# Kernel optimization log

Hardware: AMD Instinct MI355X
Metric: run time of the kernel (lower is better)

## Reference

```python
import jax, jax.numpy as jnp
import numpy as np

B, C, L, T = 8, 512, 2048, 64

def setup_inputs() -> dict:
    key = jax.random.key(0)
    k1, k2, k3 = jax.random.split(key, 3)
    x = jax.random.normal(k1, (B, C, 1, L), dtype=jnp.float32)
    W1 = jax.random.normal(k2, (T, C), dtype=jnp.float32) * (1.0 / np.sqrt(C))
    W2 = jax.random.normal(k3, (T, C), dtype=jnp.float32) * (1.0 / np.sqrt(C))
    gamma = jnp.ones((1, 1), dtype=jnp.float32)
    ranges = 0  # unused by forward
    return {"x": x, "W1": W1, "W2": W2, "gamma": gamma, "ranges": ranges}

def reference(x, W1, W2, gamma, ranges):
    temp = x[:, :, 0, :]                                  # (B, C, L)
    q = jnp.einsum('tc,bcl->btl', W1, temp)               # conv1x1 -> (B, T, L)
    k = jnp.einsum('tc,bcl->btl', W2, temp)               # conv1x1 -> (B, T, L)
    scores = jnp.einsum('btl,btm->blm', q, k)             # Q^T K -> (B, L, L)
    attn = jax.nn.softmax(scores, axis=2)                 # softmax over last dim
    # temp @ attn^T: out[:, :, j] = sum_i attn[j, i] * temp[:, :, i]
    out = jnp.einsum('bci,bji->bcj', temp, attn)          # (B, C, L)
    out = temp + gamma[0, 0] * out                        # gamma scale + residual
    return out[:, :, None, :]                             # (B, C, 1, L)
```

## Files before the change

kernel.cpp:

```cpp
#include <hip/hip_runtime.h>
#include <cstddef>

#define BB 8
#define CC 512
#define LL 2048
#define TT 64

typedef short short8 __attribute__((ext_vector_type(8)));
typedef float floatx4 __attribute__((ext_vector_type(4)));
typedef unsigned short b16u;
typedef unsigned int u32;

static __device__ __forceinline__ unsigned f2bfu(float f) {
    unsigned u = __float_as_uint(f);
    u += 0x7fffu + ((u >> 16) & 1u);
    return u >> 16;
}
static __device__ __forceinline__ float bfu2f(unsigned h) {
    return __uint_as_float(h << 16);
}

#define MFMA16(a, b, c) __builtin_amdgcn_mfma_f32_16x16x32_bf16((a), (b), (c), 0, 0, 0)

static __device__ __forceinline__ void gl2lds16(const void* g, void* l) {
    __builtin_amdgcn_global_load_lds(
        (const __attribute__((address_space(1))) u32*)g,
        (__attribute__((address_space(3))) u32*)l, 16, 0, 0);
}

__global__ __launch_bounds__(256) void wcvt_kernel(
    const float* __restrict__ W1, const float* __restrict__ W2,
    b16u* __restrict__ W1h, b16u* __restrict__ W1l,
    b16u* __restrict__ W2h, b16u* __restrict__ W2l)
{
    int flat = blockIdx.x * 256 + threadIdx.x;
    float4 v1 = *(const float4*)(W1 + (size_t)flat * 4);
    float4 v2 = *(const float4*)(W2 + (size_t)flat * 4);
    const float* e1 = (const float*)&v1;
    const float* e2 = (const float*)&v2;
    unsigned h1[4], l1[4], h2[4], l2[4];
#pragma unroll
    for (int k = 0; k < 4; ++k) {
        h1[k] = f2bfu(e1[k]); l1[k] = f2bfu(e1[k] - bfu2f(h1[k]));
        h2[k] = f2bfu(e2[k]); l2[k] = f2bfu(e2[k] - bfu2f(h2[k]));
    }
    uint2 a, b, c, d;
    a.x = h1[0] | (h1[1] << 16); a.y = h1[2] | (h1[3] << 16);
    b.x = l1[0] | (l1[1] << 16); b.y = l1[2] | (l1[3] << 16);
    c.x = h2[0] | (h2[1] << 16); c.y = h2[2] | (h2[3] << 16);
    d.x = l2[0] | (l2[1] << 16); d.y = l2[2] | (l2[3] << 16);
    *(uint2*)(W1h + (size_t)flat * 4) = a;
    *(uint2*)(W1l + (size_t)flat * 4) = b;
    *(uint2*)(W2h + (size_t)flat * 4) = c;
    *(uint2*)(W2l + (size_t)flat * 4) = d;
}

__global__ __launch_bounds__(256) void qkcvt_kernel(
    const float* __restrict__ x,
    const b16u* __restrict__ W1h, const b16u* __restrict__ W1l,
    const b16u* __restrict__ W2h, const b16u* __restrict__ W2l,
    b16u* __restrict__ Qt, b16u* __restrict__ Kt, b16u* __restrict__ XT)
{
    __shared__ b16u Sxh[64 * 72];
    __shared__ b16u Sxl[64 * 72];
    __shared__ b16u S1h[64 * 72];
    __shared__ b16u S1l[64 * 72];
    __shared__ b16u S2h[64 * 72];
    __shared__ b16u S2l[64 * 72];
    const int b  = blockIdx.y;
    const int lt = blockIdx.x;
    const int l0 = lt * 64;
    const int tid = threadIdx.x;
    const int lane = tid & 63;
    const int w = tid >> 6;
    const int n16 = lane & 15;
    const int qd = lane >> 4;
    const float* xb = x + (size_t)b * CC * LL;

    const int cx = tid >> 2;
    const int sx = tid & 3;

    float4 xreg[4];
#pragma unroll
    for (int p = 0; p < 4; ++p)
        xreg[p] = *(const float4*)(xb + (size_t)cx * LL + l0 + (sx * 4 + p) * 4);

    floatx4 aq[4], ak[4];
#pragma unroll
    for (int nt = 0; nt < 4; ++nt) {
        aq[nt] = (floatx4){0.f, 0.f, 0.f, 0.f};
        ak[nt] = (floatx4){0.f, 0.f, 0.f, 0.f};
    }

    for (int c0 = 0; c0 < 512; c0 += 64) {
        __syncthreads();
#pragma unroll
        for (int p = 0; p < 4; ++p) {
            const float* e = (const float*)&xreg[p];
            int s = sx * 4 + p;
            int lbase = s * 4;
            unsigned h[4];
#pragma unroll
            for (int k = 0; k < 4; ++k) {
                h[k] = f2bfu(e[k]);
                unsigned lo = f2bfu(e[k] - bfu2f(h[k]));
                Sxh[(lbase + k) * 72 + cx] = (b16u)h[k];
                Sxl[(lbase + k) * 72 + cx] = (b16u)lo;
            }
            uint2 wv;
            wv.x = h[0] | (h[1] << 16);
            wv.y = h[2] | (h[3] << 16);
            int phys = (((s >> 1) ^ (cx & 7)) << 3) + ((s & 1) << 2);
            *(uint2*)(XT + (((size_t)(b * 32) + lt) * 512 + c0 + cx) * 64 + phys) = wv;
        }
#pragma unroll
        for (int p = 0; p < 2; ++p) {
            int flat = tid + p * 256;
            int t = flat >> 3, s8 = flat & 7;
            size_t off = (size_t)t * 512 + c0 + s8 * 8;
            *(uint4*)&S1h[t * 72 + s8 * 8] = *(const uint4*)(W1h + off);
            *(uint4*)&S1l[t * 72 + s8 * 8] = *(const uint4*)(W1l + off);
            *(uint4*)&S2h[t * 72 + s8 * 8] = *(const uint4*)(W2h + off);
            *(uint4*)&S2l[t * 72 + s8 * 8] = *(const uint4*)(W2l + off);
        }
        __syncthreads();
        if (c0 < 448) {
#pragma unroll
            for (int p = 0; p < 4; ++p)
                xreg[p] = *(const float4*)(xb + (size_t)(c0 + 64 + cx) * LL +
                                           l0 + (sx * 4 + p) * 4);
        }
#pragma unroll
        for (int kc = 0; kc < 2; ++kc) {
            const int ao = (w * 16 + n16) * 72 + kc * 32 + qd * 8;
            short8 a1h = *(const short8*)&S1h[ao];
            short8 a1l = *(const short8*)&S1l[ao];
            short8 a2h = *(const short8*)&S2h[ao];
            short8 a2l = *(const short8*)&S2l[ao];
#pragma unroll
            for (int nt = 0; nt < 4; ++nt) {
                const int bo = (nt * 16 + n16) * 72 + kc * 32 + qd * 8;
                short8 bh = *(const short8*)&Sxh[bo];
                short8 bl = *(const short8*)&Sxl[bo];
                aq[nt] = MFMA16(a1h, bh, aq[nt]);
                aq[nt] = MFMA16(a1h, bl, aq[nt]);
                aq[nt] = MFMA16(a1l, bh, aq[nt]);
                ak[nt] = MFMA16(a2h, bh, ak[nt]);
                ak[nt] = MFMA16(a2h, bl, ak[nt]);
                ak[nt] = MFMA16(a2l, bh, ak[nt]);
            }
        }
    }
#pragma unroll
    for (int nt = 0; nt < 4; ++nt) {
        int l = l0 + nt * 16 + n16;
        uint2 pq, pk;
        pq.x = f2bfu(aq[nt][0]) | (f2bfu(aq[nt][1]) << 16);
        pq.y = f2bfu(aq[nt][2]) | (f2bfu(aq[nt][3]) << 16);
        pk.x = f2bfu(ak[nt][0]) | (f2bfu(ak[nt][1]) << 16);
        pk.y = f2bfu(ak[nt][2]) | (f2bfu(ak[nt][3]) << 16);
        *(uint2*)(Qt + ((size_t)(b * 2048) + l) * 64 + w * 16 + qd * 4) = pq;
        *(uint2*)(Kt + ((size_t)(b * 2048) + l) * 64 + w * 16 + qd * 4) = pk;
    }
}

__global__ __launch_bounds__(256) void pexp_kernel(
    const b16u* __restrict__ Qt, const b16u* __restrict__ Kt,
    b16u* __restrict__ P, float* __restrict__ Zpart, int b_off)
{
    __shared__ b16u Ks[64 * 72];
    __shared__ b16u Ls[64 * 68];
    __shared__ float Zw[4][64];
    const int pb = blockIdx.z, b = b_off + pb;
    const int j0 = blockIdx.y * 64;
    const int ibase = blockIdx.x * 512;
    const int tid = threadIdx.x;
    const int lane = tid & 63;
    const int w = tid >> 6;
    const int n16 = lane & 15;
    const int qd = lane >> 4;
    const b16u* kb = Kt + (size_t)b * (2048 * 64);

    short8 qf[4][2];
#pragma unroll
    for (int nt = 0; nt < 4; ++nt)
#pragma unroll
        for (int kc = 0; kc < 2; ++kc)
            qf[nt][kc] = *(const short8*)(Qt +
                ((size_t)(b * 2048) + j0 + nt * 16 + n16) * 64 + kc * 32 + qd * 8);

    uint4 kreg[2];
#pragma unroll
    for (int p = 0; p < 2; ++p) {
        int flat = tid + p * 256;
        kreg[p] = *(const uint4*)(kb + (size_t)(ibase + (flat >> 3)) * 64 + (flat & 7) * 8);
    }
    float zacc[4] = {0.f, 0.f, 0.f, 0.f};

    for (int it = 0; it < 8; ++it) {
#pragma unroll
        for (int p = 0; p < 2; ++p) {
            int flat = tid + p * 256;
            *(uint4*)&Ks[(flat >> 3) * 72 + (flat & 7) * 8] = kreg[p];
        }
        {
            const int itn = (it + 1 < 8) ? it + 1 : 7;
#pragma unroll
            for (int p = 0; p < 2; ++p) {
                int flat = tid + p * 256;
                kreg[p] = *(const uint4*)(kb +
                    (size_t)(ibase + itn * 64 + (flat >> 3)) * 64 + (flat & 7) * 8);
            }
        }
        __syncthreads();
        floatx4 sacc[4];
#pragma unroll
        for (int nt = 0; nt < 4; ++nt) sacc[nt] = (floatx4){0.f, 0.f, 0.f, 0.f};
#pragma unroll
        for (int kc = 0; kc < 2; ++kc) {
            short8 af = *(const short8*)&Ks[(w * 16 + n16) * 72 + kc * 32 + qd * 8];
#pragma unroll
            for (int nt = 0; nt < 4; ++nt)
                sacc[nt] = MFMA16(af, qf[nt][kc], sacc[nt]);
        }
#pragma unroll
        for (int nt = 0; nt < 4; ++nt) {
            float p0 = __expf(sacc[nt][0] - 20.0f);
            float p1 = __expf(sacc[nt][1] - 20.0f);
            float p2 = __expf(sacc[nt][2] - 20.0f);
            float p3 = __expf(sacc[nt][3] - 20.0f);
            zacc[nt] += (p0 + p1) + (p2 + p3);
            uint2 pk;
            pk.x = f2bfu(p0) | (f2bfu(p1) << 16);
            pk.y = f2bfu(p2) | (f2bfu(p3) << 16);
            *(uint2*)&Ls[(nt * 16 + n16) * 68 + w * 16 + qd * 4] = pk;
        }
        __syncthreads();
        size_t prow = ((size_t)(pb * 32) + (ibase >> 6) + it) * 2048 + j0;
#pragma unroll
        for (int p = 0; p < 4; ++p) {
            int u = tid + p * 256;
            int row = u >> 4, s = u & 15;
            int phys = (((s >> 1) ^ (row & 7)) << 3) + ((s & 1) << 2);
            *(uint2*)(P + (prow + row) * 64 + phys) = *(const uint2*)&Ls[row * 68 + s * 4];
        }
    }
#pragma unroll
    for (int nt = 0; nt < 4; ++nt) {
        float z = zacc[nt];
        z += __shfl_xor(z, 16);
        z += __shfl_xor(z, 32);
        if (qd == 0) Zw[w][nt * 16 + n16] = z;
    }
    __syncthreads();
    if (tid < 64) {
        float s = Zw[0][tid] + Zw[1][tid] + Zw[2][tid] + Zw[3][tid];
        Zpart[((size_t)blockIdx.x * 8 + b) * 2048 + j0 + tid] = s;
    }
}

__global__ __launch_bounds__(128) void gemm_kernel(
    const float* __restrict__ x, const b16u* __restrict__ XT,
    const b16u* __restrict__ P, const float* __restrict__ Zpart,
    const float* __restrict__ gamma, float* __restrict__ out, int b_off)
{
    __shared__ __align__(16) char smem[49152];
    b16u* As = (b16u*)smem;
    b16u* Bs = (b16u*)(smem + 32768);
    const int pb = blockIdx.z, b = b_off + pb;
    const int j0 = blockIdx.x * 64;
    const int c0 = blockIdx.y * 128;
    const int tid = threadIdx.x;
    const int lane = tid & 63;
    const int w = tid >> 6;
    const int n16 = lane & 15;
    const int qd = lane >> 4;

    const b16u* tA = XT + ((size_t)(b * 32) * 512 + c0) * 64 + w * 4096 + lane * 8;
    const b16u* tB = P + ((size_t)(pb * 32) * 2048 + j0) * 64 + w * 2048 + lane * 8;
    b16u* lA = As + w * 4096;
    b16u* lB = Bs + w * 2048;

#define STAGE(IT, BUF)                                                    \
    {                                                                      \
        const b16u* ga = tA + (size_t)(IT) * 32768;                        \
        const b16u* gb = tB + (size_t)(IT) * 131072;                       \
        _Pragma("unroll")                                                  \
        for (int ch = 0; ch < 8; ++ch)                                     \
            gl2lds16(ga + ch * 512, lA + (BUF) * 8192 + ch * 512);         \
        _Pragma("unroll")                                                  \
        for (int ch = 0; ch < 4; ++ch)                                     \
            gl2lds16(gb + ch * 512, lB + (BUF) * 4096 + ch * 512);         \
    }

    STAGE(0, 0)
    __syncthreads();

    floatx4 acc[4][4];
#pragma unroll
    for (int mt = 0; mt < 4; ++mt)
#pragma unroll
        for (int nt = 0; nt < 4; ++nt) acc[mt][nt] = (floatx4){0.f, 0.f, 0.f, 0.f};

    for (int it = 0; it < 32; ++it) {
        const int buf = it & 1;
        if (it < 31) STAGE(it + 1, buf ^ 1)
        const b16u* Ab = As + buf * 8192;
        const b16u* Bb = Bs + buf * 4096;
#pragma unroll
        for (int kc = 0; kc < 2; ++kc) {
            const int co = (((kc * 4 + qd) ^ (n16 & 7)) << 3);
            short8 af[4], bf[4];
#pragma unroll
            for (int mt = 0; mt < 4; ++mt)
                af[mt] = *(const short8*)&Ab[(w * 64 + mt * 16 + n16) * 64 + co];
#pragma unroll
            for (int nt = 0; nt < 4; ++nt)
                bf[nt] = *(const short8*)&Bb[(nt * 16 + n16) * 64 + co];
#pragma unroll
            for (int mt = 0; mt < 4; ++mt)
#pragma unroll
                for (int nt = 0; nt < 4; ++nt)
                    acc[mt][nt] = MFMA16(af[mt], bf[nt], acc[mt][nt]);
        }
        __syncthreads();
    }
#undef STAGE

    const float g = gamma[0];
    float* st = (float*)(smem + w * 17408);
#pragma unroll
    for (int nt = 0; nt < 4; ++nt) {
        int j = j0 + nt * 16 + n16;
        float zsum = Zpart[(size_t)b * 2048 + j]
                   + Zpart[(size_t)(1 * 8 + b) * 2048 + j]
                   + Zpart[(size_t)(2 * 8 + b) * 2048 + j]
                   + Zpart[(size_t)(3 * 8 + b) * 2048 + j];
        float zi = g / zsum;
#pragma unroll
        for (int mt = 0; mt < 4; ++mt)
#pragma unroll
            for (int r = 0; r < 4; ++r)
                st[(mt * 16 + qd * 4 + r) * 68 + nt * 16 + n16] = acc[mt][nt][r] * zi;
    }
    __syncthreads();
#pragma unroll
    for (int p = 0; p < 16; ++p) {
        int rl = p * 4 + qd;
        int cg = c0 + w * 64 + rl;
        size_t go = ((size_t)(b * 512) + cg) * 2048 + j0 + n16 * 4;
        float4 v = *(const float4*)&st[rl * 68 + n16 * 4];
        float4 xv = *(const float4*)(x + go);
        v.x += xv.x; v.y += xv.y; v.z += xv.z; v.w += xv.w;
        *(float4*)(out + go) = v;
    }
}

extern "C" void kernel_launch(void* const* d_in, const int* in_sizes, int n_in,
                              void* d_out, int out_size, void* d_ws, size_t ws_size,
                              hipStream_t stream)
{
    const float* x     = (const float*)d_in[0];
    const float* W1    = (const float*)d_in[1];
    const float* W2    = (const float*)d_in[2];
    const float* gamma = (const float*)d_in[3];
    float* out = (float*)d_out;

    b16u* Qt  = (b16u*)d_ws;
    b16u* Kt  = Qt  + (size_t)BB * LL * TT;
    b16u* W1h = Kt  + (size_t)BB * LL * TT;
    b16u* W1l = W1h + (size_t)TT * CC;
    b16u* W2h = W1l + (size_t)TT * CC;
    b16u* W2l = W2h + (size_t)TT * CC;
    float* Zp = (float*)(W2l + (size_t)TT * CC);
    b16u* XT  = (b16u*)(Zp + 4 * 8 * 2048);
    b16u* P   = XT + (size_t)BB * 32 * 512 * 64;

    const size_t base = (size_t)((char*)P - (char*)d_ws);
    const size_t pbat = (size_t)LL * LL * 2;
    int nb = 8;
    if (ws_size < base + 8 * pbat) nb = 4;
    if (ws_size < base + 4 * pbat) nb = 2;
    if (ws_size < base + 2 * pbat) nb = 1;

    wcvt_kernel <<<dim3(32),     256, 0, stream>>>(W1, W2, W1h, W1l, W2h, W2l);
    qkcvt_kernel<<<dim3(32, BB), 256, 0, stream>>>(x, W1h, W1l, W2h, W2l, Qt, Kt, XT);
    for (int b0 = 0; b0 < BB; b0 += nb) {
        pexp_kernel<<<dim3(4, 32, nb), 256, 0, stream>>>(Qt, Kt, P, Zp, b0);
        gemm_kernel<<<dim3(32, 4, nb), 128, 0, stream>>>(x, XT, P, Zp, gamma, out, b0);
    }
}
```

Before: 198.3 us.

## Enlarge gemm tile to 128x128 with four waves in a 2x2 layout

The output GEMM block now covers 128 channels by 128 positions using four waves arranged 2x2 instead of two waves over a 128x64 tile. The grid is flattened so that the four channel blocks sharing the same P columns are adjacent, which should improve L2 reuse of the large P matrix. This halves the number of blocks and raises arithmetic intensity per LDS byte, at the cost of more LDS (about 68 KB) and fewer blocks in flight, with the launch bound set to two blocks per CU. The epilogue row mapping is also changed to match the new wave layout.

```diff
diff --git a/kernel.cpp b/kernel.cpp
--- a/kernel.cpp
+++ b/kernel.cpp
@@ -259,26 +259,29 @@
     }
 }
 
-__global__ __launch_bounds__(128) void gemm_kernel(
+__global__ __launch_bounds__(256, 2) void gemm_kernel(
     const float* __restrict__ x, const b16u* __restrict__ XT,
     const b16u* __restrict__ P, const float* __restrict__ Zpart,
     const float* __restrict__ gamma, float* __restrict__ out, int b_off)
 {
-    __shared__ __align__(16) char smem[49152];
+    __shared__ __align__(16) char smem[69632];
     b16u* As = (b16u*)smem;
     b16u* Bs = (b16u*)(smem + 32768);
-    const int pb = blockIdx.z, b = b_off + pb;
-    const int j0 = blockIdx.x * 64;
-    const int c0 = blockIdx.y * 128;
+    const int pb = blockIdx.y, b = b_off + pb;
+    const int id = blockIdx.x;
+    const int c0 = (id & 3) * 128;
+    const int j0 = (id >> 2) * 128;
     const int tid = threadIdx.x;
     const int lane = tid & 63;
     const int w = tid >> 6;
     const int n16 = lane & 15;
     const int qd = lane >> 4;
-
-    const b16u* tA = XT + ((size_t)(b * 32) * 512 + c0) * 64 + w * 4096 + lane * 8;
+    const int wc = w & 1;
+    const int wj = w >> 1;
+
+    const b16u* tA = XT + ((size_t)(b * 32) * 512 + c0) * 64 + w * 2048 + lane * 8;
     const b16u* tB = P + ((size_t)(pb * 32) * 2048 + j0) * 64 + w * 2048 + lane * 8;
-    b16u* lA = As + w * 4096;
+    b16u* lA = As + w * 2048;
     b16u* lB = Bs + w * 2048;
 
 #define STAGE(IT, BUF)                                                    \
@@ -286,11 +289,10 @@
         const b16u* ga = tA + (size_t)(IT) * 32768;                        \
         const b16u* gb = tB + (size_t)(IT) * 131072;                       \
         _Pragma("unroll")                                                  \
-        for (int ch = 0; ch < 8; ++ch)                                     \
+        for (int ch = 0; ch < 4; ++ch) {                                   \
             gl2lds16(ga + ch * 512, lA + (BUF) * 8192 + ch * 512);         \
-        _Pragma("unroll")                                                  \
-        for (int ch = 0; ch < 4; ++ch)                                     \
-            gl2lds16(gb + ch * 512, lB + (BUF) * 4096 + ch * 512);         \
+            gl2lds16(gb + ch * 512, lB + (BUF) * 8192 + ch * 512);         \
+        }                                                                  \
     }
 
     STAGE(0, 0)
@@ -306,17 +308,17 @@
         const int buf = it & 1;
         if (it < 31) STAGE(it + 1, buf ^ 1)
         const b16u* Ab = As + buf * 8192;
-        const b16u* Bb = Bs + buf * 4096;
+        const b16u* Bb = Bs + buf * 8192;
 #pragma unroll
         for (int kc = 0; kc < 2; ++kc) {
             const int co = (((kc * 4 + qd) ^ (n16 & 7)) << 3);
             short8 af[4], bf[4];
 #pragma unroll
             for (int mt = 0; mt < 4; ++mt)
-                af[mt] = *(const short8*)&Ab[(w * 64 + mt * 16 + n16) * 64 + co];
+                af[mt] = *(const short8*)&Ab[(wc * 64 + mt * 16 + n16) * 64 + co];
 #pragma unroll
             for (int nt = 0; nt < 4; ++nt)
-                bf[nt] = *(const short8*)&Bb[(nt * 16 + n16) * 64 + co];
+                bf[nt] = *(const short8*)&Bb[(wj * 64 + nt * 16 + n16) * 64 + co];
 #pragma unroll
             for (int mt = 0; mt < 4; ++mt)
 #pragma unroll
@@ -331,7 +333,7 @@
     float* st = (float*)(smem + w * 17408);
 #pragma unroll
     for (int nt = 0; nt < 4; ++nt) {
-        int j = j0 + nt * 16 + n16;
+        int j = j0 + wj * 64 + nt * 16 + n16;
         float zsum = Zpart[(size_t)b * 2048 + j]
                    + Zpart[(size_t)(1 * 8 + b) * 2048 + j]
                    + Zpart[(size_t)(2 * 8 + b) * 2048 + j]
@@ -346,9 +348,9 @@
     __syncthreads();
 #pragma unroll
     for (int p = 0; p < 16; ++p) {
-        int rl = p * 4 + qd;
-        int cg = c0 + w * 64 + rl;
-        size_t go = ((size_t)(b * 512) + cg) * 2048 + j0 + n16 * 4;
+        int rl = qd * 16 + p;
+        int cg = c0 + wc * 64 + rl;
+        size_t go = ((size_t)(b * 512) + cg) * 2048 + j0 + wj * 64 + n16 * 4;
         float4 v = *(const float4*)&st[rl * 68 + n16 * 4];
         float4 xv = *(const float4*)(x + go);
         v.x += xv.x; v.y += xv.y; v.z += xv.z; v.w += xv.w;
@@ -387,6 +389,6 @@
     qkcvt_kernel<<<dim3(32, BB), 256, 0, stream>>>(x, W1h, W1l, W2h, W2l, Qt, Kt, XT);
     for (int b0 = 0; b0 < BB; b0 += nb) {
         pexp_kernel<<<dim3(4, 32, nb), 256, 0, stream>>>(Qt, Kt, P, Zp, b0);
-        gemm_kernel<<<dim3(32, 4, nb), 128, 0, stream>>>(x, XT, P, Zp, gamma, out, b0);
-    }
-}
+        gemm_kernel<<<dim3(64, nb),    256, 0, stream>>>(x, XT, P, Zp, gamma, out, b0);
+    }
+}
```

Measured after the change: 182.4 us. 8.0% less time.
